# Kernel optimization log

Hardware: AMD Instinct MI355X
Metric: run time of the kernel (lower is better)

Reference implementation:

```python
import jax, jax.numpy as jnp
import numpy as np

B, N, F, H, D = 2, 2048, 1024, 16, 64


def setup_inputs() -> dict:
    key = jax.random.key(0)
    ks = jax.random.split(key, 5)
    s = 0.02
    return {
        "x": jax.random.normal(ks[0], (B, N, F), jnp.float32),
        "w_qkv": (jax.random.normal(ks[1], (3 * H * D, F), jnp.float32) * s),
        "w_out": (jax.random.normal(ks[2], (F, H * D), jnp.float32) * s),
        "w_hp_pre": (jax.random.normal(ks[3], (H, H), jnp.float32) * (1.0 / H)),
        "b_hp_pre": jnp.zeros((H,), jnp.float32),
        "w_hp_post": (jax.random.normal(ks[4], (H, H), jnp.float32) * (1.0 / H)),
        "b_hp_post": jnp.zeros((H,), jnp.float32),
    }


def reference(x, w_qkv, w_out, w_hp_pre, b_hp_pre, w_hp_post, b_hp_post):
    b, n, f = x.shape
    # qkv projection; rearrange 'b n (h d qkv) -> qkv b h n d' (qkv innermost)
    proj = (x @ w_qkv.T).reshape(b, n, H, D, 3)
    q = jnp.transpose(proj[..., 0], (0, 2, 1, 3))  # b h n d
    k = jnp.transpose(proj[..., 1], (0, 2, 1, 3))
    v = jnp.transpose(proj[..., 2], (0, 2, 1, 3))
    kv = jnp.stack([k, v], axis=0)  # (2, b, h, n, d) -- returned cache

    scale = D ** -0.5
    dots = jnp.einsum('bhid,bhjd->bhij', q, k) * scale
    # pre talking-heads: 1x1 conv over head channel
    dots = jnp.einsum('gh,bhij->bgij', w_hp_pre, dots) + b_hp_pre[None, :, None, None]
    attn = jax.nn.softmax(dots, axis=-1)
    # post talking-heads
    attn = jnp.einsum('gh,bhij->bgij', w_hp_post, attn) + b_hp_post[None, :, None, None]
    out = jnp.einsum('bhij,bhjd->bhid', attn, v)
    out = jnp.transpose(out, (0, 2, 1, 3)).reshape(b, n, H * D)
    out = out @ w_out.T
    return out, kv
```

## Files before the change

### kernel.cpp

```cpp
#include <hip/hip_runtime.h>
#include <hip/hip_bf16.h>
#include <cstdint>
#include <cstddef>

#define B_ 2
#define N_ 2048
#define F_ 1024
#define H_ 16
#define D_ 64

typedef float f32x4 __attribute__((ext_vector_type(4)));
typedef short s16x8 __attribute__((ext_vector_type(8)));
typedef short s16x4 __attribute__((ext_vector_type(4)));

__device__ __forceinline__ unsigned short f2bf(float f) {
  union { __hip_bfloat16 h; unsigned short u; } c;
  c.h = __float2bfloat16(f);
  return c.u;
}
__device__ __forceinline__ float bf2f(unsigned short u) {
  union { __hip_bfloat16 h; unsigned short u; } c;
  c.u = u;
  return __bfloat162float(c.h);
}

__global__ __launch_bounds__(256) void cvt_bf16(const float* __restrict__ in,
                                                unsigned short* __restrict__ out,
                                                int n8) {
  const int t = blockIdx.x * 256 + threadIdx.x;
  if (t >= n8) return;
  const float4* p = (const float4*)in + (size_t)t * 2;
  float4 a = p[0], b = p[1];
  s16x8 o;
  o[0] = f2bf(a.x); o[1] = f2bf(a.y); o[2] = f2bf(a.z); o[3] = f2bf(a.w);
  o[4] = f2bf(b.x); o[5] = f2bf(b.y); o[6] = f2bf(b.z); o[7] = f2bf(b.w);
  *((s16x8*)out + t) = o;
}

__global__ __launch_bounds__(256) void cvt_wqkv_perm(const float* __restrict__ in,
                                                     unsigned short* __restrict__ out) {
  const int t = blockIdx.x * 256 + threadIdx.x;
  const int rowp = t >> 7;
  const int kk = (t & 127) * 8;
  const int c = rowp >> 10, rem = rowp & 1023;
  const int h = rem >> 6, d = rem & 63;
  const float* p = in + (size_t)(h * 192 + d * 3 + c) * 1024 + kk;
  float4 a = *(const float4*)p, b = *(const float4*)(p + 4);
  s16x8 o;
  o[0] = f2bf(a.x); o[1] = f2bf(a.y); o[2] = f2bf(a.z); o[3] = f2bf(a.w);
  o[4] = f2bf(b.x); o[5] = f2bf(b.y); o[6] = f2bf(b.z); o[7] = f2bf(b.w);
  *((s16x8*)&out[(size_t)rowp * 1024 + kk]) = o;
}

__global__ __launch_bounds__(256) void cvt_sum4(const float* __restrict__ a,
                                                unsigned short* __restrict__ out) {
  const int t = blockIdx.x * 256 + threadIdx.x;
  const size_t stride = (size_t)B_ * N_ * 1024 / 4;
  float4 x0 = *((const float4*)a + t);
  float4 x1 = *((const float4*)a + stride + t);
  float4 x2 = *((const float4*)a + 2 * stride + t);
  float4 x3 = *((const float4*)a + 3 * stride + t);
  s16x4 o;
  o[0] = f2bf((x0.x + x1.x) + (x2.x + x3.x));
  o[1] = f2bf((x0.y + x1.y) + (x2.y + x3.y));
  o[2] = f2bf((x0.z + x1.z) + (x2.z + x3.z));
  o[3] = f2bf((x0.w + x1.w) + (x2.w + x3.w));
  *((s16x4*)out + t) = o;
}

template <int MODE>
__global__ __launch_bounds__(256) void gemm_bf16(const unsigned short* __restrict__ A,
                                                 const unsigned short* __restrict__ W,
                                                 float* __restrict__ o0,
                                                 unsigned short* __restrict__ oQ,
                                                 unsigned short* __restrict__ oK,
                                                 unsigned short* __restrict__ oVt) {
  __shared__ unsigned short As[128 * 72];
  __shared__ unsigned short Bs[128 * 72];
  const int m0 = blockIdx.y * 128, c0 = blockIdx.x * 128;
  const int tid = threadIdx.x;
  const int wave = tid >> 6, lane = tid & 63;
  const int wm = (wave & 1) * 64, wn = (wave >> 1) * 64;
  const int lm = lane & 15, lq = lane >> 4;
  f32x4 acc[4][4] = {};
  for (int k0 = 0; k0 < 1024; k0 += 64) {
#pragma unroll
    for (int it = 0; it < 4; ++it) {
      const int chunk = it * 256 + tid;
      const int row = chunk >> 3, kq = (chunk & 7) * 8;
      *(float4*)&As[row * 72 + kq] = *(const float4*)&A[(size_t)(m0 + row) * 1024 + k0 + kq];
      *(float4*)&Bs[row * 72 + kq] = *(const float4*)&W[(size_t)(c0 + row) * 1024 + k0 + kq];
    }
    __syncthreads();
#pragma unroll
    for (int ks = 0; ks < 2; ++ks) {
      s16x8 af[4], bfr[4];
#pragma unroll
      for (int i = 0; i < 4; ++i) {
        af[i] = *(const s16x8*)&As[(wm + i * 16 + lm) * 72 + ks * 32 + lq * 8];
        bfr[i] = *(const s16x8*)&Bs[(wn + i * 16 + lm) * 72 + ks * 32 + lq * 8];
      }
#pragma unroll
      for (int i = 0; i < 4; ++i)
#pragma unroll
        for (int j = 0; j < 4; ++j)
          acc[i][j] = __builtin_amdgcn_mfma_f32_16x16x32_bf16(af[i], bfr[j], acc[i][j], 0, 0, 0);
    }
    __syncthreads();
  }
  if (MODE == 1) {
#pragma unroll
    for (int i = 0; i < 4; ++i)
#pragma unroll
      for (int j = 0; j < 4; ++j)
#pragma unroll
        for (int r = 0; r < 4; ++r) {
          const int m = m0 + wm + i * 16 + lq * 4 + r;
          const int col = c0 + wn + j * 16 + lm;
          o0[(size_t)m * 1024 + col] = acc[i][j][r];
        }
  } else {
    const int cls = blockIdx.x >> 3;
    const int colbase = (blockIdx.x & 7) * 128;
    if (cls == 0) {
#pragma unroll
      for (int i = 0; i < 4; ++i)
#pragma unroll
        for (int j = 0; j < 4; ++j) {
          const int cl = colbase + wn + j * 16 + lm;
          const int h = cl >> 6, d = cl & 63;
#pragma unroll
          for (int r = 0; r < 4; ++r) {
            const int m = m0 + wm + i * 16 + lq * 4 + r;
            const int bb = m >> 11, n = m & 2047;
            oQ[(((size_t)bb * H_ + h) * N_ + n) * D_ + d] = f2bf(acc[i][j][r]);
          }
        }
    } else if (cls == 1) {
#pragma unroll
      for (int i = 0; i < 4; ++i)
#pragma unroll
        for (int j = 0; j < 4; ++j) {
          const int cl = colbase + wn + j * 16 + lm;
          const int h = cl >> 6, d = cl & 63;
#pragma unroll
          for (int r = 0; r < 4; ++r) {
            const int m = m0 + wm + i * 16 + lq * 4 + r;
            const int bb = m >> 11, n = m & 2047;
            const size_t idx = (((size_t)bb * H_ + h) * N_ + n) * D_ + d;
            o0[idx] = acc[i][j][r];
            oK[idx] = f2bf(acc[i][j][r]);
          }
        }
    } else {
#pragma unroll
      for (int i = 0; i < 4; ++i) {
        const int n0 = m0 + wm + i * 16 + lq * 4;
        const int bb = n0 >> 11, nl = n0 & 2047;
#pragma unroll
        for (int j = 0; j < 4; ++j) {
          const int cl = colbase + wn + j * 16 + lm;
          const int h = cl >> 6, d = cl & 63;
          s16x4 vp;
#pragma unroll
          for (int r = 0; r < 4; ++r) {
            const size_t idx = (((size_t)bb * H_ + h) * N_ + nl + r) * D_ + d;
            o0[(size_t)B_ * H_ * N_ * D_ + idx] = acc[i][j][r];
            vp[r] = (short)f2bf(acc[i][j][r]);
          }
          *(s16x4*)&oVt[(((size_t)bb * H_ + h) * D_ + d) * N_ + nl] = vp;
        }
      }
    }
  }
}

#define SS_J 20
#define SLOT 320
#define SS_I 644
#define PS_J 36
#define PS_G 1156

__global__ __launch_bounds__(512) void attn_l(const unsigned short* __restrict__ Qb,
                                              const unsigned short* __restrict__ Kb,
                                              const float* __restrict__ wpre,
                                              const float* __restrict__ bpre,
                                              float* __restrict__ l_glob) {
  __shared__ unsigned short Ssh[32 * SS_I];
  const int tid = threadIdx.x;
  const int wave = tid >> 6, lane = tid & 63;
  const int lm = lane & 15, lq = lane >> 4;
  const int b = blockIdx.z, jh = blockIdx.y;
  const int i0 = blockIdx.x * 32;
  const int j00 = jh * 512;
  const int h0 = wave * 2;

  s16x8 aq[2][2][2];
#pragma unroll
  for (int hh = 0; hh < 2; ++hh)
#pragma unroll
    for (int mi = 0; mi < 2; ++mi)
#pragma unroll
      for (int ks = 0; ks < 2; ++ks)
        aq[hh][mi][ks] = *(const s16x8*)&Qb[(((size_t)(b * H_ + h0 + hh) * N_) + i0 + mi * 16 + lm) * D_ + ks * 32 + lq * 8];

  s16x8 apre;
#pragma unroll
  for (int t = 0; t < 8; ++t) apre[t] = 0;
  if (lq < 2)
#pragma unroll
    for (int t = 0; t < 8; ++t) apre[t] = (short)f2bf(wpre[lm * 16 + lq * 8 + t] * 0.125f);
  float bpre_r[4];
#pragma unroll
  for (int r = 0; r < 4; ++r) bpre_r[r] = bpre[lq * 4 + r];

  float lacc[4][4] = {};

  for (int js = 0; js < 512; js += 32) {
    const int j0 = j00 + js;
    __syncthreads();
#pragma unroll
    for (int jt = 0; jt < 2; ++jt) {
      f32x4 c[2][2];
#pragma unroll
      for (int hh = 0; hh < 2; ++hh) {
        const unsigned short* kp = &Kb[(((size_t)(b * H_ + h0 + hh) * N_) + j0 + jt * 16 + lm) * D_ + lq * 8];
        s16x8 b0 = *(const s16x8*)kp;
        s16x8 b1 = *(const s16x8*)(kp + 32);
#pragma unroll
        for (int mi = 0; mi < 2; ++mi) {
          f32x4 cc = {};
          cc = __builtin_amdgcn_mfma_f32_16x16x32_bf16(aq[hh][mi][0], b0, cc, 0, 0, 0);
          cc = __builtin_amdgcn_mfma_f32_16x16x32_bf16(aq[hh][mi][1], b1, cc, 0, 0, 0);
          c[hh][mi] = cc;
        }
      }
#pragma unroll
      for (int mi = 0; mi < 2; ++mi)
#pragma unroll
        for (int r = 0; r < 4; ++r) {
          unsigned int pk = (unsigned int)f2bf(c[0][mi][r]) | ((unsigned int)f2bf(c[1][mi][r]) << 16);
          *(unsigned int*)&Ssh[(mi * 16 + lq * 4 + r) * SS_I + jt * SLOT + lm * SS_J + h0] = pk;
        }
    }
    __syncthreads();
#pragma unroll
    for (int ii = 0; ii < 8; ++ii) {
      const int i_loc = wave * 4 + (ii & 3), jt = ii >> 2;
      const unsigned short* srow = &Ssh[i_loc * SS_I + jt * SLOT];
      s16x8 bs;
#pragma unroll
      for (int t = 0; t < 8; ++t) bs[t] = 0;
      if (lq < 2) {
        s16x4 p0 = *(const s16x4*)(srow + lm * SS_J + lq * 8);
        s16x4 p1 = *(const s16x4*)(srow + lm * SS_J + lq * 8 + 4);
        bs[0] = p0[0]; bs[1] = p0[1]; bs[2] = p0[2]; bs[3] = p0[3];
        bs[4] = p1[0]; bs[5] = p1[1]; bs[6] = p1[2]; bs[7] = p1[3];
      }
      f32x4 c = {};
      c = __builtin_amdgcn_mfma_f32_16x16x32_bf16(apre, bs, c, 0, 0, 0);
#pragma unroll
      for (int r = 0; r < 4; ++r) lacc[ii & 3][r] += __expf(c[r] + bpre_r[r]);
    }
  }
#pragma unroll
  for (int ig = 0; ig < 4; ++ig)
#pragma unroll
    for (int r = 0; r < 4; ++r) {
      float v = lacc[ig][r];
      v += __shfl_xor(v, 1); v += __shfl_xor(v, 2);
      v += __shfl_xor(v, 4); v += __shfl_xor(v, 8);
      if (lm == 0)
        atomicAdd(&l_glob[((size_t)b * N_ + i0 + wave * 4 + ig) * H_ + lq * 4 + r], v);
    }
}

__global__ __launch_bounds__(512) void attn_av(const unsigned short* __restrict__ Qb,
                                               const unsigned short* __restrict__ Kb,
                                               const unsigned short* __restrict__ Vt,
                                               const float* __restrict__ wpre,
                                               const float* __restrict__ bpre,
                                               const float* __restrict__ wpost,
                                               const float* __restrict__ bpost,
                                               const float* __restrict__ l_glob,
                                               float* __restrict__ Opart) {
  __shared__ unsigned short Ssh[32 * SS_I];
  __shared__ unsigned short Psh[16 * PS_G];
  __shared__ float linv[512];
  const int tid = threadIdx.x;
  const int wave = tid >> 6, lane = tid & 63;
  const int lm = lane & 15, lq = lane >> 4;
  const int b = blockIdx.z, jh = blockIdx.y;
  const int i0 = blockIdx.x * 32;
  const int j00 = jh * 512;
  const int h0 = wave * 2;
  float* Oout = Opart + (size_t)jh * ((size_t)B_ * N_ * 1024);

  linv[tid] = 1.0f / l_glob[((size_t)b * N_ + i0 + (tid >> 4)) * H_ + (tid & 15)];

  s16x8 aq[2][2][2];
#pragma unroll
  for (int hh = 0; hh < 2; ++hh)
#pragma unroll
    for (int mi = 0; mi < 2; ++mi)
#pragma unroll
      for (int ks = 0; ks < 2; ++ks)
        aq[hh][mi][ks] = *(const s16x8*)&Qb[(((size_t)(b * H_ + h0 + hh) * N_) + i0 + mi * 16 + lm) * D_ + ks * 32 + lq * 8];

  s16x8 apre, apost;
#pragma unroll
  for (int t = 0; t < 8; ++t) { apre[t] = 0; apost[t] = 0; }
  if (lq < 2)
#pragma unroll
    for (int t = 0; t < 8; ++t) {
      apre[t] = (short)f2bf(wpre[lm * 16 + lq * 8 + t] * 0.125f);
      apost[t] = (short)f2bf(wpost[lm * 16 + lq * 8 + t]);
    }
  float bpre_r[4];
#pragma unroll
  for (int r = 0; r < 4; ++r) bpre_r[r] = bpre[lq * 4 + r];
  const float bpost_lm = bpost[lm];

  f32x4 acc[2][2][4] = {};

  for (int js = 0; js < 512; js += 32) {
    const int j0 = j00 + js;
#pragma unroll
    for (int jt = 0; jt < 2; ++jt) {
      f32x4 c[2][2];
#pragma unroll
      for (int hh = 0; hh < 2; ++hh) {
        const unsigned short* kp = &Kb[(((size_t)(b * H_ + h0 + hh) * N_) + j0 + jt * 16 + lm) * D_ + lq * 8];
        s16x8 b0 = *(const s16x8*)kp;
        s16x8 b1 = *(const s16x8*)(kp + 32);
#pragma unroll
        for (int mi = 0; mi < 2; ++mi) {
          f32x4 cc = {};
          cc = __builtin_amdgcn_mfma_f32_16x16x32_bf16(aq[hh][mi][0], b0, cc, 0, 0, 0);
          cc = __builtin_amdgcn_mfma_f32_16x16x32_bf16(aq[hh][mi][1], b1, cc, 0, 0, 0);
          c[hh][mi] = cc;
        }
      }
#pragma unroll
      for (int mi = 0; mi < 2; ++mi)
#pragma unroll
        for (int r = 0; r < 4; ++r) {
          unsigned int pk = (unsigned int)f2bf(c[0][mi][r]) | ((unsigned int)f2bf(c[1][mi][r]) << 16);
          *(unsigned int*)&Ssh[(mi * 16 + lq * 4 + r) * SS_I + jt * SLOT + lm * SS_J + h0] = pk;
        }
    }
    __syncthreads();
#pragma unroll
    for (int ii = 0; ii < 8; ++ii) {
      const int i_loc = wave * 4 + (ii & 3), jt = ii >> 2;
      unsigned short* srow = &Ssh[i_loc * SS_I + jt * SLOT];
      s16x8 bs;
#pragma unroll
      for (int t = 0; t < 8; ++t) bs[t] = 0;
      if (lq < 2) {
        s16x4 p0 = *(const s16x4*)(srow + lm * SS_J + lq * 8);
        s16x4 p1 = *(const s16x4*)(srow + lm * SS_J + lq * 8 + 4);
        bs[0] = p0[0]; bs[1] = p0[1]; bs[2] = p0[2]; bs[3] = p0[3];
        bs[4] = p1[0]; bs[5] = p1[1]; bs[6] = p1[2]; bs[7] = p1[3];
      }
      f32x4 c = {};
      c = __builtin_amdgcn_mfma_f32_16x16x32_bf16(apre, bs, c, 0, 0, 0);
      const float4 li = *(const float4*)&linv[i_loc * 16 + lq * 4];
      const float lif[4] = {li.x, li.y, li.z, li.w};
      s16x4 ep;
#pragma unroll
      for (int r = 0; r < 4; ++r)
        ep[r] = (short)f2bf(__expf(c[r] + bpre_r[r]) * lif[r]);
      *(s16x4*)(srow + lm * SS_J + lq * 4) = ep;
      s16x8 be;
#pragma unroll
      for (int t = 0; t < 8; ++t) be[t] = 0;
      if (lq < 2) {
        s16x4 q0 = *(const s16x4*)(srow + lm * SS_J + lq * 8);
        s16x4 q1 = *(const s16x4*)(srow + lm * SS_J + lq * 8 + 4);
        be[0] = q0[0]; be[1] = q0[1]; be[2] = q0[2]; be[3] = q0[3];
        be[4] = q1[0]; be[5] = q1[1]; be[6] = q1[2]; be[7] = q1[3];
      }
      f32x4 c2 = {};
      c2 = __builtin_amdgcn_mfma_f32_16x16x32_bf16(be, apost, c2, 0, 0, 0);
      s16x4 pv;
#pragma unroll
      for (int r = 0; r < 4; ++r) pv[r] = (short)f2bf(c2[r] + bpost_lm);
      *(s16x4*)&Psh[lm * PS_G + i_loc * PS_J + jt * 16 + lq * 4] = pv;
    }
    __syncthreads();
#pragma unroll
    for (int g = 0; g < 2; ++g) {
      const int gg = h0 + g;
      s16x8 bv[4];
#pragma unroll
      for (int nd = 0; nd < 4; ++nd)
        bv[nd] = *(const s16x8*)&Vt[(((size_t)(b * H_ + gg) * D_) + nd * 16 + lm) * N_ + j0 + lq * 8];
#pragma unroll
      for (int mi = 0; mi < 2; ++mi) {
        const unsigned short* pb = &Psh[gg * PS_G + (mi * 16 + lm) * PS_J + lq * 8];
        s16x4 a0 = *(const s16x4*)pb;
        s16x4 a1 = *(const s16x4*)(pb + 4);
        s16x8 ap;
        ap[0] = a0[0]; ap[1] = a0[1]; ap[2] = a0[2]; ap[3] = a0[3];
        ap[4] = a1[0]; ap[5] = a1[1]; ap[6] = a1[2]; ap[7] = a1[3];
#pragma unroll
        for (int nd = 0; nd < 4; ++nd)
          acc[g][mi][nd] = __builtin_amdgcn_mfma_f32_16x16x32_bf16(ap, bv[nd], acc[g][mi][nd], 0, 0, 0);
      }
    }
  }
#pragma unroll
  for (int g = 0; g < 2; ++g)
#pragma unroll
    for (int mi = 0; mi < 2; ++mi)
#pragma unroll
      for (int nd = 0; nd < 4; ++nd)
#pragma unroll
        for (int r = 0; r < 4; ++r)
          Oout[((size_t)b * N_ + i0 + mi * 16 + lq * 4 + r) * 1024 + (h0 + g) * 64 + nd * 16 + lm] = acc[g][mi][nd][r];
}

extern "C" void kernel_launch(void* const* d_in, const int* in_sizes, int n_in,
                              void* d_out, int out_size, void* d_ws,
                              size_t ws_size, hipStream_t stream) {
  (void)in_sizes; (void)n_in; (void)out_size; (void)ws_size;
  const float* x      = (const float*)d_in[0];
  const float* w_qkv  = (const float*)d_in[1];
  const float* w_out  = (const float*)d_in[2];
  const float* w_pre  = (const float*)d_in[3];
  const float* b_pre  = (const float*)d_in[4];
  const float* w_post = (const float*)d_in[5];
  const float* b_post = (const float*)d_in[6];

  float* out = (float*)d_out;
  float* kv  = out + (size_t)B_ * N_ * F_;

  unsigned short* xb  = (unsigned short*)d_ws;
  unsigned short* wqb = xb + (size_t)4096 * 1024;
  unsigned short* wob = wqb + (size_t)3072 * 1024;
  unsigned short* Qb  = wob + (size_t)1024 * 1024;
  unsigned short* Kb  = Qb + (size_t)B_ * H_ * N_ * D_;
  unsigned short* Vt  = Kb + (size_t)B_ * H_ * N_ * D_;
  unsigned short* O1  = Vt + (size_t)B_ * H_ * N_ * D_;
  float* l_glob = (float*)(O1 + (size_t)B_ * N_ * F_);
  float* Oh = l_glob + (size_t)B_ * N_ * H_;

  cvt_bf16<<<dim3(4096 * 1024 / 8 / 256), 256, 0, stream>>>(x, xb, 4096 * 1024 / 8);
  cvt_wqkv_perm<<<dim3(3072 * 128 / 256), 256, 0, stream>>>(w_qkv, wqb);
  cvt_bf16<<<dim3(1024 * 1024 / 8 / 256), 256, 0, stream>>>(w_out, wob, 1024 * 1024 / 8);
  hipMemsetAsync(l_glob, 0, (size_t)B_ * N_ * H_ * 4, stream);

  gemm_bf16<0><<<dim3(3072 / 128, 4096 / 128), 256, 0, stream>>>(xb, wqb, kv, Qb, Kb, Vt);

  attn_l<<<dim3(N_ / 32, 4, B_), 512, 0, stream>>>(Qb, Kb, w_pre, b_pre, l_glob);
  attn_av<<<dim3(N_ / 32, 4, B_), 512, 0, stream>>>(Qb, Kb, Vt, w_pre, b_pre, w_post, b_post,
                                                    l_glob, Oh);

  cvt_sum4<<<dim3(B_ * N_ * F_ / 4 / 256), 256, 0, stream>>>(Oh, O1);

  gemm_bf16<1><<<dim3(1024 / 128, 4096 / 128), 256, 0, stream>>>(O1, wob, out, nullptr, nullptr, nullptr);
}
```

Before: 440.0 us.

## Halve attention query tile to 16 rows and raise occupancy with zero-padded LDS

Both attention kernels now process 16 query rows per block instead of 32, doubling the grid, shrinking LDS and register footprint, and requesting four blocks per CU via launch bounds. The talking-heads MFMA operands are no longer zeroed conditionally per lane: the LDS score buffer is zero-initialized once, so all lanes load unconditionally. LDS reads, MFMAs and exps are batched into separate phases. The aim is better latency hiding through occupancy, at the cost of reloading K and V tiles twice as often per query row.

```diff
diff --git a/kernel.cpp b/kernel.cpp
--- a/kernel.cpp
+++ b/kernel.cpp
@@ -178,31 +178,32 @@
 #define SS_J 20
 #define SLOT 320
 #define SS_I 644
+#define SS_TOT (16 * SS_I + 16)
 #define PS_J 36
-#define PS_G 1156
-
-__global__ __launch_bounds__(512) void attn_l(const unsigned short* __restrict__ Qb,
-                                              const unsigned short* __restrict__ Kb,
-                                              const float* __restrict__ wpre,
-                                              const float* __restrict__ bpre,
-                                              float* __restrict__ l_glob) {
-  __shared__ unsigned short Ssh[32 * SS_I];
+#define PS_G 580
+
+__global__ __launch_bounds__(512, 4) void attn_l(const unsigned short* __restrict__ Qb,
+                                                 const unsigned short* __restrict__ Kb,
+                                                 const float* __restrict__ wpre,
+                                                 const float* __restrict__ bpre,
+                                                 float* __restrict__ l_glob) {
+  __shared__ unsigned short Ssh[SS_TOT];
   const int tid = threadIdx.x;
   const int wave = tid >> 6, lane = tid & 63;
   const int lm = lane & 15, lq = lane >> 4;
   const int b = blockIdx.z, jh = blockIdx.y;
-  const int i0 = blockIdx.x * 32;
+  const int i0 = blockIdx.x * 16;
   const int j00 = jh * 512;
   const int h0 = wave * 2;
 
-  s16x8 aq[2][2][2];
+  for (int t = tid; t < SS_TOT; t += 512) Ssh[t] = 0;
+
+  s16x8 aq[2][2];
 #pragma unroll
   for (int hh = 0; hh < 2; ++hh)
 #pragma unroll
-    for (int mi = 0; mi < 2; ++mi)
-#pragma unroll
-      for (int ks = 0; ks < 2; ++ks)
-        aq[hh][mi][ks] = *(const s16x8*)&Qb[(((size_t)(b * H_ + h0 + hh) * N_) + i0 + mi * 16 + lm) * D_ + ks * 32 + lq * 8];
+    for (int ks = 0; ks < 2; ++ks)
+      aq[hh][ks] = *(const s16x8*)&Qb[(((size_t)(b * H_ + h0 + hh) * N_) + i0 + lm) * D_ + ks * 32 + lq * 8];
 
   s16x8 apre;
 #pragma unroll
@@ -214,98 +215,92 @@
 #pragma unroll
   for (int r = 0; r < 4; ++r) bpre_r[r] = bpre[lq * 4 + r];
 
-  float lacc[4][4] = {};
+  float lacc[2][4] = {};
 
   for (int js = 0; js < 512; js += 32) {
     const int j0 = j00 + js;
     __syncthreads();
 #pragma unroll
     for (int jt = 0; jt < 2; ++jt) {
-      f32x4 c[2][2];
+      f32x4 c[2];
 #pragma unroll
       for (int hh = 0; hh < 2; ++hh) {
         const unsigned short* kp = &Kb[(((size_t)(b * H_ + h0 + hh) * N_) + j0 + jt * 16 + lm) * D_ + lq * 8];
         s16x8 b0 = *(const s16x8*)kp;
         s16x8 b1 = *(const s16x8*)(kp + 32);
-#pragma unroll
-        for (int mi = 0; mi < 2; ++mi) {
-          f32x4 cc = {};
-          cc = __builtin_amdgcn_mfma_f32_16x16x32_bf16(aq[hh][mi][0], b0, cc, 0, 0, 0);
-          cc = __builtin_amdgcn_mfma_f32_16x16x32_bf16(aq[hh][mi][1], b1, cc, 0, 0, 0);
-          c[hh][mi] = cc;
-        }
-      }
-#pragma unroll
-      for (int mi = 0; mi < 2; ++mi)
-#pragma unroll
-        for (int r = 0; r < 4; ++r) {
-          unsigned int pk = (unsigned int)f2bf(c[0][mi][r]) | ((unsigned int)f2bf(c[1][mi][r]) << 16);
-          *(unsigned int*)&Ssh[(mi * 16 + lq * 4 + r) * SS_I + jt * SLOT + lm * SS_J + h0] = pk;
-        }
-    }
-    __syncthreads();
-#pragma unroll
-    for (int ii = 0; ii < 8; ++ii) {
-      const int i_loc = wave * 4 + (ii & 3), jt = ii >> 2;
-      const unsigned short* srow = &Ssh[i_loc * SS_I + jt * SLOT];
+        f32x4 cc = {};
+        cc = __builtin_amdgcn_mfma_f32_16x16x32_bf16(aq[hh][0], b0, cc, 0, 0, 0);
+        cc = __builtin_amdgcn_mfma_f32_16x16x32_bf16(aq[hh][1], b1, cc, 0, 0, 0);
+        c[hh] = cc;
+      }
+#pragma unroll
+      for (int r = 0; r < 4; ++r) {
+        unsigned int pk = (unsigned int)f2bf(c[0][r]) | ((unsigned int)f2bf(c[1][r]) << 16);
+        *(unsigned int*)&Ssh[(lq * 4 + r) * SS_I + jt * SLOT + lm * SS_J + h0] = pk;
+      }
+    }
+    __syncthreads();
+    s16x4 p0[4], p1[4];
+#pragma unroll
+    for (int ii = 0; ii < 4; ++ii) {
+      const unsigned short* srow = &Ssh[(wave * 2 + (ii & 1)) * SS_I + (ii >> 1) * SLOT + lm * SS_J + lq * 8];
+      p0[ii] = *(const s16x4*)srow;
+      p1[ii] = *(const s16x4*)(srow + 4);
+    }
+#pragma unroll
+    for (int ii = 0; ii < 4; ++ii) {
       s16x8 bs;
-#pragma unroll
-      for (int t = 0; t < 8; ++t) bs[t] = 0;
-      if (lq < 2) {
-        s16x4 p0 = *(const s16x4*)(srow + lm * SS_J + lq * 8);
-        s16x4 p1 = *(const s16x4*)(srow + lm * SS_J + lq * 8 + 4);
-        bs[0] = p0[0]; bs[1] = p0[1]; bs[2] = p0[2]; bs[3] = p0[3];
-        bs[4] = p1[0]; bs[5] = p1[1]; bs[6] = p1[2]; bs[7] = p1[3];
-      }
+      bs[0] = p0[ii][0]; bs[1] = p0[ii][1]; bs[2] = p0[ii][2]; bs[3] = p0[ii][3];
+      bs[4] = p1[ii][0]; bs[5] = p1[ii][1]; bs[6] = p1[ii][2]; bs[7] = p1[ii][3];
       f32x4 c = {};
       c = __builtin_amdgcn_mfma_f32_16x16x32_bf16(apre, bs, c, 0, 0, 0);
 #pragma unroll
-      for (int r = 0; r < 4; ++r) lacc[ii & 3][r] += __expf(c[r] + bpre_r[r]);
+      for (int r = 0; r < 4; ++r) lacc[ii & 1][r] += __expf(c[r] + bpre_r[r]);
     }
   }
 #pragma unroll
-  for (int ig = 0; ig < 4; ++ig)
+  for (int ig = 0; ig < 2; ++ig)
 #pragma unroll
     for (int r = 0; r < 4; ++r) {
       float v = lacc[ig][r];
       v += __shfl_xor(v, 1); v += __shfl_xor(v, 2);
       v += __shfl_xor(v, 4); v += __shfl_xor(v, 8);
       if (lm == 0)
-        atomicAdd(&l_glob[((size_t)b * N_ + i0 + wave * 4 + ig) * H_ + lq * 4 + r], v);
-    }
-}
-
-__global__ __launch_bounds__(512) void attn_av(const unsigned short* __restrict__ Qb,
-                                               const unsigned short* __restrict__ Kb,
-                                               const unsigned short* __restrict__ Vt,
-                                               const float* __restrict__ wpre,
-                                               const float* __restrict__ bpre,
-                                               const float* __restrict__ wpost,
-                                               const float* __restrict__ bpost,
-                                               const float* __restrict__ l_glob,
-                                               float* __restrict__ Opart) {
-  __shared__ unsigned short Ssh[32 * SS_I];
+        atomicAdd(&l_glob[((size_t)b * N_ + i0 + wave * 2 + ig) * H_ + lq * 4 + r], v);
+    }
+}
+
+__global__ __launch_bounds__(512, 4) void attn_av(const unsigned short* __restrict__ Qb,
+                                                  const unsigned short* __restrict__ Kb,
+                                                  const unsigned short* __restrict__ Vt,
+                                                  const float* __restrict__ wpre,
+                                                  const float* __restrict__ bpre,
+                                                  const float* __restrict__ wpost,
+                                                  const float* __restrict__ bpost,
+                                                  const float* __restrict__ l_glob,
+                                                  float* __restrict__ Opart) {
+  __shared__ unsigned short Ssh[SS_TOT];
   __shared__ unsigned short Psh[16 * PS_G];
-  __shared__ float linv[512];
+  __shared__ float linv[256];
   const int tid = threadIdx.x;
   const int wave = tid >> 6, lane = tid & 63;
   const int lm = lane & 15, lq = lane >> 4;
   const int b = blockIdx.z, jh = blockIdx.y;
-  const int i0 = blockIdx.x * 32;
+  const int i0 = blockIdx.x * 16;
   const int j00 = jh * 512;
   const int h0 = wave * 2;
   float* Oout = Opart + (size_t)jh * ((size_t)B_ * N_ * 1024);
 
-  linv[tid] = 1.0f / l_glob[((size_t)b * N_ + i0 + (tid >> 4)) * H_ + (tid & 15)];
-
-  s16x8 aq[2][2][2];
+  for (int t = tid; t < SS_TOT; t += 512) Ssh[t] = 0;
+  if (tid < 256)
+    linv[tid] = 1.0f / l_glob[((size_t)b * N_ + i0 + (tid >> 4)) * H_ + (tid & 15)];
+
+  s16x8 aq[2][2];
 #pragma unroll
   for (int hh = 0; hh < 2; ++hh)
 #pragma unroll
-    for (int mi = 0; mi < 2; ++mi)
-#pragma unroll
-      for (int ks = 0; ks < 2; ++ks)
-        aq[hh][mi][ks] = *(const s16x8*)&Qb[(((size_t)(b * H_ + h0 + hh) * N_) + i0 + mi * 16 + lm) * D_ + ks * 32 + lq * 8];
+    for (int ks = 0; ks < 2; ++ks)
+      aq[hh][ks] = *(const s16x8*)&Qb[(((size_t)(b * H_ + h0 + hh) * N_) + i0 + lm) * D_ + ks * 32 + lq * 8];
 
   s16x8 apre, apost;
 #pragma unroll
@@ -321,72 +316,82 @@
   for (int r = 0; r < 4; ++r) bpre_r[r] = bpre[lq * 4 + r];
   const float bpost_lm = bpost[lm];
 
-  f32x4 acc[2][2][4] = {};
+  __syncthreads();
+
+  float lifs[2][4];
+#pragma unroll
+  for (int u = 0; u < 2; ++u)
+#pragma unroll
+    for (int r = 0; r < 4; ++r)
+      lifs[u][r] = linv[(wave * 2 + u) * 16 + lq * 4 + r];
+
+  f32x4 acc[2][4] = {};
 
   for (int js = 0; js < 512; js += 32) {
     const int j0 = j00 + js;
 #pragma unroll
     for (int jt = 0; jt < 2; ++jt) {
-      f32x4 c[2][2];
+      f32x4 c[2];
 #pragma unroll
       for (int hh = 0; hh < 2; ++hh) {
         const unsigned short* kp = &Kb[(((size_t)(b * H_ + h0 + hh) * N_) + j0 + jt * 16 + lm) * D_ + lq * 8];
         s16x8 b0 = *(const s16x8*)kp;
         s16x8 b1 = *(const s16x8*)(kp + 32);
-#pragma unroll
-        for (int mi = 0; mi < 2; ++mi) {
-          f32x4 cc = {};
-          cc = __builtin_amdgcn_mfma_f32_16x16x32_bf16(aq[hh][mi][0], b0, cc, 0, 0, 0);
-          cc = __builtin_amdgcn_mfma_f32_16x16x32_bf16(aq[hh][mi][1], b1, cc, 0, 0, 0);
-          c[hh][mi] = cc;
-        }
-      }
-#pragma unroll
-      for (int mi = 0; mi < 2; ++mi)
-#pragma unroll
-        for (int r = 0; r < 4; ++r) {
-          unsigned int pk = (unsigned int)f2bf(c[0][mi][r]) | ((unsigned int)f2bf(c[1][mi][r]) << 16);
-          *(unsigned int*)&Ssh[(mi * 16 + lq * 4 + r) * SS_I + jt * SLOT + lm * SS_J + h0] = pk;
-        }
-    }
-    __syncthreads();
-#pragma unroll
-    for (int ii = 0; ii < 8; ++ii) {
-      const int i_loc = wave * 4 + (ii & 3), jt = ii >> 2;
-      unsigned short* srow = &Ssh[i_loc * SS_I + jt * SLOT];
+        f32x4 cc = {};
+        cc = __builtin_amdgcn_mfma_f32_16x16x32_bf16(aq[hh][0], b0, cc, 0, 0, 0);
+        cc = __builtin_amdgcn_mfma_f32_16x16x32_bf16(aq[hh][1], b1, cc, 0, 0, 0);
+        c[hh] = cc;
+      }
+#pragma unroll
+      for (int r = 0; r < 4; ++r) {
+        unsigned int pk = (unsigned int)f2bf(c[0][r]) | ((unsigned int)f2bf(c[1][r]) << 16);
+        *(unsigned int*)&Ssh[(lq * 4 + r) * SS_I + jt * SLOT + lm * SS_J + h0] = pk;
+      }
+    }
+    __syncthreads();
+    s16x4 p0[4], p1[4];
+#pragma unroll
+    for (int ii = 0; ii < 4; ++ii) {
+      const unsigned short* srow = &Ssh[(wave * 2 + (ii & 1)) * SS_I + (ii >> 1) * SLOT + lm * SS_J + lq * 8];
+      p0[ii] = *(const s16x4*)srow;
+      p1[ii] = *(const s16x4*)(srow + 4);
+    }
+    f32x4 cpre[4];
+#pragma unroll
+    for (int ii = 0; ii < 4; ++ii) {
       s16x8 bs;
-#pragma unroll
-      for (int t = 0; t < 8; ++t) bs[t] = 0;
-      if (lq < 2) {
-        s16x4 p0 = *(const s16x4*)(srow + lm * SS_J + lq * 8);
-        s16x4 p1 = *(const s16x4*)(srow + lm * SS_J + lq * 8 + 4);
-        bs[0] = p0[0]; bs[1] = p0[1]; bs[2] = p0[2]; bs[3] = p0[3];
-        bs[4] = p1[0]; bs[5] = p1[1]; bs[6] = p1[2]; bs[7] = p1[3];
-      }
+      bs[0] = p0[ii][0]; bs[1] = p0[ii][1]; bs[2] = p0[ii][2]; bs[3] = p0[ii][3];
+      bs[4] = p1[ii][0]; bs[5] = p1[ii][1]; bs[6] = p1[ii][2]; bs[7] = p1[ii][3];
       f32x4 c = {};
-      c = __builtin_amdgcn_mfma_f32_16x16x32_bf16(apre, bs, c, 0, 0, 0);
-      const float4 li = *(const float4*)&linv[i_loc * 16 + lq * 4];
-      const float lif[4] = {li.x, li.y, li.z, li.w};
+      cpre[ii] = __builtin_amdgcn_mfma_f32_16x16x32_bf16(apre, bs, c, 0, 0, 0);
+    }
+#pragma unroll
+    for (int ii = 0; ii < 4; ++ii) {
+      unsigned short* srow = &Ssh[(wave * 2 + (ii & 1)) * SS_I + (ii >> 1) * SLOT];
       s16x4 ep;
 #pragma unroll
       for (int r = 0; r < 4; ++r)
-        ep[r] = (short)f2bf(__expf(c[r] + bpre_r[r]) * lif[r]);
+        ep[r] = (short)f2bf(__expf(cpre[ii][r] + bpre_r[r]) * lifs[ii & 1][r]);
       *(s16x4*)(srow + lm * SS_J + lq * 4) = ep;
+    }
+    s16x4 q0[4], q1[4];
+#pragma unroll
+    for (int ii = 0; ii < 4; ++ii) {
+      const unsigned short* srow = &Ssh[(wave * 2 + (ii & 1)) * SS_I + (ii >> 1) * SLOT + lm * SS_J + lq * 8];
+      q0[ii] = *(const s16x4*)srow;
+      q1[ii] = *(const s16x4*)(srow + 4);
+    }
+#pragma unroll
+    for (int ii = 0; ii < 4; ++ii) {
       s16x8 be;
-#pragma unroll
-      for (int t = 0; t < 8; ++t) be[t] = 0;
-      if (lq < 2) {
-        s16x4 q0 = *(const s16x4*)(srow + lm * SS_J + lq * 8);
-        s16x4 q1 = *(const s16x4*)(srow + lm * SS_J + lq * 8 + 4);
-        be[0] = q0[0]; be[1] = q0[1]; be[2] = q0[2]; be[3] = q0[3];
-        be[4] = q1[0]; be[5] = q1[1]; be[6] = q1[2]; be[7] = q1[3];
-      }
+      be[0] = q0[ii][0]; be[1] = q0[ii][1]; be[2] = q0[ii][2]; be[3] = q0[ii][3];
+      be[4] = q1[ii][0]; be[5] = q1[ii][1]; be[6] = q1[ii][2]; be[7] = q1[ii][3];
       f32x4 c2 = {};
       c2 = __builtin_amdgcn_mfma_f32_16x16x32_bf16(be, apost, c2, 0, 0, 0);
       s16x4 pv;
 #pragma unroll
       for (int r = 0; r < 4; ++r) pv[r] = (short)f2bf(c2[r] + bpost_lm);
-      *(s16x4*)&Psh[lm * PS_G + i_loc * PS_J + jt * 16 + lq * 4] = pv;
+      *(s16x4*)&Psh[lm * PS_G + (wave * 2 + (ii & 1)) * PS_J + (ii >> 1) * 16 + lq * 4] = pv;
     }
     __syncthreads();
 #pragma unroll
@@ -396,29 +401,24 @@
 #pragma unroll
       for (int nd = 0; nd < 4; ++nd)
         bv[nd] = *(const s16x8*)&Vt[(((size_t)(b * H_ + gg) * D_) + nd * 16 + lm) * N_ + j0 + lq * 8];
-#pragma unroll
-      for (int mi = 0; mi < 2; ++mi) {
-        const unsigned short* pb = &Psh[gg * PS_G + (mi * 16 + lm) * PS_J + lq * 8];
-        s16x4 a0 = *(const s16x4*)pb;
-        s16x4 a1 = *(const s16x4*)(pb + 4);
-        s16x8 ap;
-        ap[0] = a0[0]; ap[1] = a0[1]; ap[2] = a0[2]; ap[3] = a0[3];
-        ap[4] = a1[0]; ap[5] = a1[1]; ap[6] = a1[2]; ap[7] = a1[3];
-#pragma unroll
-        for (int nd = 0; nd < 4; ++nd)
-          acc[g][mi][nd] = __builtin_amdgcn_mfma_f32_16x16x32_bf16(ap, bv[nd], acc[g][mi][nd], 0, 0, 0);
-      }
+      const unsigned short* pb = &Psh[gg * PS_G + lm * PS_J + lq * 8];
+      s16x4 a0 = *(const s16x4*)pb;
+      s16x4 a1 = *(const s16x4*)(pb + 4);
+      s16x8 ap;
+      ap[0] = a0[0]; ap[1] = a0[1]; ap[2] = a0[2]; ap[3] = a0[3];
+      ap[4] = a1[0]; ap[5] = a1[1]; ap[6] = a1[2]; ap[7] = a1[3];
+#pragma unroll
+      for (int nd = 0; nd < 4; ++nd)
+        acc[g][nd] = __builtin_amdgcn_mfma_f32_16x16x32_bf16(ap, bv[nd], acc[g][nd], 0, 0, 0);
     }
   }
 #pragma unroll
   for (int g = 0; g < 2; ++g)
 #pragma unroll
-    for (int mi = 0; mi < 2; ++mi)
-#pragma unroll
-      for (int nd = 0; nd < 4; ++nd)
-#pragma unroll
-        for (int r = 0; r < 4; ++r)
-          Oout[((size_t)b * N_ + i0 + mi * 16 + lq * 4 + r) * 1024 + (h0 + g) * 64 + nd * 16 + lm] = acc[g][mi][nd][r];
+    for (int nd = 0; nd < 4; ++nd)
+#pragma unroll
+      for (int r = 0; r < 4; ++r)
+        Oout[((size_t)b * N_ + i0 + lq * 4 + r) * 1024 + (h0 + g) * 64 + nd * 16 + lm] = acc[g][nd][r];
 }
 
 extern "C" void kernel_launch(void* const* d_in, const int* in_sizes, int n_in,
@@ -453,8 +453,8 @@
 
   gemm_bf16<0><<<dim3(3072 / 128, 4096 / 128), 256, 0, stream>>>(xb, wqb, kv, Qb, Kb, Vt);
 
-  attn_l<<<dim3(N_ / 32, 4, B_), 512, 0, stream>>>(Qb, Kb, w_pre, b_pre, l_glob);
-  attn_av<<<dim3(N_ / 32, 4, B_), 512, 0, stream>>>(Qb, Kb, Vt, w_pre, b_pre, w_post, b_post,
+  attn_l<<<dim3(N_ / 16, 4, B_), 512, 0, stream>>>(Qb, Kb, w_pre, b_pre, l_glob);
+  attn_av<<<dim3(N_ / 16, 4, B_), 512, 0, stream>>>(Qb, Kb, Vt, w_pre, b_pre, w_post, b_post,
                                                     l_glob, Oh);
 
   cvt_sum4<<<dim3(B_ * N_ * F_ / 4 / 256), 256, 0, stream>>>(Oh, O1);
```

After: 549.6 us. 1.25x slower.

## Raise occupancy in attention kernels by reloading Q and batching LDS reads

Applied to the files above, without the earlier changes.

Drops the register-resident Q fragments and reloads them from global memory inside the inner loop, and adds launch_bounds min-block hints (6 and 4) to cut register use and raise occupancy. The shared S buffer is padded and zero-filled up front so the lq>=2 lanes can read it unconditionally, removing the branchy zeroing. The pre/post talking-head loops are restructured to batch four LDS reads before the MFMAs, exposing more instruction-level parallelism. The cost is extra global/L2 traffic for Q on every tile and possible register spills under the tighter bounds.

```diff
diff --git a/kernel.cpp b/kernel.cpp
--- a/kernel.cpp
+++ b/kernel.cpp
@@ -178,15 +178,16 @@
 #define SS_J 20
 #define SLOT 320
 #define SS_I 644
+#define SS_TOT (32 * SS_I + 16)
 #define PS_J 36
 #define PS_G 1156
 
-__global__ __launch_bounds__(512) void attn_l(const unsigned short* __restrict__ Qb,
-                                              const unsigned short* __restrict__ Kb,
-                                              const float* __restrict__ wpre,
-                                              const float* __restrict__ bpre,
-                                              float* __restrict__ l_glob) {
-  __shared__ unsigned short Ssh[32 * SS_I];
+__global__ __launch_bounds__(512, 6) void attn_l(const unsigned short* __restrict__ Qb,
+                                                 const unsigned short* __restrict__ Kb,
+                                                 const float* __restrict__ wpre,
+                                                 const float* __restrict__ bpre,
+                                                 float* __restrict__ l_glob) {
+  __shared__ unsigned short Ssh[SS_TOT];
   const int tid = threadIdx.x;
   const int wave = tid >> 6, lane = tid & 63;
   const int lm = lane & 15, lq = lane >> 4;
@@ -195,14 +196,7 @@
   const int j00 = jh * 512;
   const int h0 = wave * 2;
 
-  s16x8 aq[2][2][2];
-#pragma unroll
-  for (int hh = 0; hh < 2; ++hh)
-#pragma unroll
-    for (int mi = 0; mi < 2; ++mi)
-#pragma unroll
-      for (int ks = 0; ks < 2; ++ks)
-        aq[hh][mi][ks] = *(const s16x8*)&Qb[(((size_t)(b * H_ + h0 + hh) * N_) + i0 + mi * 16 + lm) * D_ + ks * 32 + lq * 8];
+  for (int t = tid; t < SS_TOT; t += 512) Ssh[t] = 0;
 
   s16x8 apre;
 #pragma unroll
@@ -229,9 +223,12 @@
         s16x8 b1 = *(const s16x8*)(kp + 32);
 #pragma unroll
         for (int mi = 0; mi < 2; ++mi) {
+          const unsigned short* qp = &Qb[(((size_t)(b * H_ + h0 + hh) * N_) + i0 + mi * 16 + lm) * D_ + lq * 8];
+          s16x8 a0 = *(const s16x8*)qp;
+          s16x8 a1 = *(const s16x8*)(qp + 32);
           f32x4 cc = {};
-          cc = __builtin_amdgcn_mfma_f32_16x16x32_bf16(aq[hh][mi][0], b0, cc, 0, 0, 0);
-          cc = __builtin_amdgcn_mfma_f32_16x16x32_bf16(aq[hh][mi][1], b1, cc, 0, 0, 0);
+          cc = __builtin_amdgcn_mfma_f32_16x16x32_bf16(a0, b0, cc, 0, 0, 0);
+          cc = __builtin_amdgcn_mfma_f32_16x16x32_bf16(a1, b1, cc, 0, 0, 0);
           c[hh][mi] = cc;
         }
       }
@@ -245,22 +242,24 @@
     }
     __syncthreads();
 #pragma unroll
-    for (int ii = 0; ii < 8; ++ii) {
-      const int i_loc = wave * 4 + (ii & 3), jt = ii >> 2;
-      const unsigned short* srow = &Ssh[i_loc * SS_I + jt * SLOT];
-      s16x8 bs;
-#pragma unroll
-      for (int t = 0; t < 8; ++t) bs[t] = 0;
-      if (lq < 2) {
-        s16x4 p0 = *(const s16x4*)(srow + lm * SS_J + lq * 8);
-        s16x4 p1 = *(const s16x4*)(srow + lm * SS_J + lq * 8 + 4);
-        bs[0] = p0[0]; bs[1] = p0[1]; bs[2] = p0[2]; bs[3] = p0[3];
-        bs[4] = p1[0]; bs[5] = p1[1]; bs[6] = p1[2]; bs[7] = p1[3];
-      }
-      f32x4 c = {};
-      c = __builtin_amdgcn_mfma_f32_16x16x32_bf16(apre, bs, c, 0, 0, 0);
-#pragma unroll
-      for (int r = 0; r < 4; ++r) lacc[ii & 3][r] += __expf(c[r] + bpre_r[r]);
+    for (int jt = 0; jt < 2; ++jt) {
+      s16x4 p0[4], p1[4];
+#pragma unroll
+      for (int u = 0; u < 4; ++u) {
+        const unsigned short* srow = &Ssh[(wave * 4 + u) * SS_I + jt * SLOT + lm * SS_J + lq * 8];
+        p0[u] = *(const s16x4*)srow;
+        p1[u] = *(const s16x4*)(srow + 4);
+      }
+#pragma unroll
+      for (int u = 0; u < 4; ++u) {
+        s16x8 bs;
+        bs[0] = p0[u][0]; bs[1] = p0[u][1]; bs[2] = p0[u][2]; bs[3] = p0[u][3];
+        bs[4] = p1[u][0]; bs[5] = p1[u][1]; bs[6] = p1[u][2]; bs[7] = p1[u][3];
+        f32x4 c = {};
+        c = __builtin_amdgcn_mfma_f32_16x16x32_bf16(apre, bs, c, 0, 0, 0);
+#pragma unroll
+        for (int r = 0; r < 4; ++r) lacc[u][r] += __expf(c[r] + bpre_r[r]);
+      }
     }
   }
 #pragma unroll
@@ -275,16 +274,16 @@
     }
 }
 
-__global__ __launch_bounds__(512) void attn_av(const unsigned short* __restrict__ Qb,
-                                               const unsigned short* __restrict__ Kb,
-                                               const unsigned short* __restrict__ Vt,
-                                               const float* __restrict__ wpre,
-                                               const float* __restrict__ bpre,
-                                               const float* __restrict__ wpost,
-                                               const float* __restrict__ bpost,
-                                               const float* __restrict__ l_glob,
-                                               float* __restrict__ Opart) {
-  __shared__ unsigned short Ssh[32 * SS_I];
+__global__ __launch_bounds__(512, 4) void attn_av(const unsigned short* __restrict__ Qb,
+                                                  const unsigned short* __restrict__ Kb,
+                                                  const unsigned short* __restrict__ Vt,
+                                                  const float* __restrict__ wpre,
+                                                  const float* __restrict__ bpre,
+                                                  const float* __restrict__ wpost,
+                                                  const float* __restrict__ bpost,
+                                                  const float* __restrict__ l_glob,
+                                                  float* __restrict__ Opart) {
+  __shared__ unsigned short Ssh[SS_TOT];
   __shared__ unsigned short Psh[16 * PS_G];
   __shared__ float linv[512];
   const int tid = threadIdx.x;
@@ -296,16 +295,8 @@
   const int h0 = wave * 2;
   float* Oout = Opart + (size_t)jh * ((size_t)B_ * N_ * 1024);
 
+  for (int t = tid; t < SS_TOT; t += 512) Ssh[t] = 0;
   linv[tid] = 1.0f / l_glob[((size_t)b * N_ + i0 + (tid >> 4)) * H_ + (tid & 15)];
-
-  s16x8 aq[2][2][2];
-#pragma unroll
-  for (int hh = 0; hh < 2; ++hh)
-#pragma unroll
-    for (int mi = 0; mi < 2; ++mi)
-#pragma unroll
-      for (int ks = 0; ks < 2; ++ks)
-        aq[hh][mi][ks] = *(const s16x8*)&Qb[(((size_t)(b * H_ + h0 + hh) * N_) + i0 + mi * 16 + lm) * D_ + ks * 32 + lq * 8];
 
   s16x8 apre, apost;
 #pragma unroll
@@ -320,6 +311,8 @@
 #pragma unroll
   for (int r = 0; r < 4; ++r) bpre_r[r] = bpre[lq * 4 + r];
   const float bpost_lm = bpost[lm];
+
+  __syncthreads();
 
   f32x4 acc[2][2][4] = {};
 
@@ -335,9 +328,12 @@
         s16x8 b1 = *(const s16x8*)(kp + 32);
 #pragma unroll
         for (int mi = 0; mi < 2; ++mi) {
+          const unsigned short* qp = &Qb[(((size_t)(b * H_ + h0 + hh) * N_) + i0 + mi * 16 + lm) * D_ + lq * 8];
+          s16x8 a0 = *(const s16x8*)qp;
+          s16x8 a1 = *(const s16x8*)(qp + 32);
           f32x4 cc = {};
-          cc = __builtin_amdgcn_mfma_f32_16x16x32_bf16(aq[hh][mi][0], b0, cc, 0, 0, 0);
-          cc = __builtin_amdgcn_mfma_f32_16x16x32_bf16(aq[hh][mi][1], b1, cc, 0, 0, 0);
+          cc = __builtin_amdgcn_mfma_f32_16x16x32_bf16(a0, b0, cc, 0, 0, 0);
+          cc = __builtin_amdgcn_mfma_f32_16x16x32_bf16(a1, b1, cc, 0, 0, 0);
           c[hh][mi] = cc;
         }
       }
@@ -351,42 +347,54 @@
     }
     __syncthreads();
 #pragma unroll
-    for (int ii = 0; ii < 8; ++ii) {
-      const int i_loc = wave * 4 + (ii & 3), jt = ii >> 2;
-      unsigned short* srow = &Ssh[i_loc * SS_I + jt * SLOT];
-      s16x8 bs;
-#pragma unroll
-      for (int t = 0; t < 8; ++t) bs[t] = 0;
-      if (lq < 2) {
-        s16x4 p0 = *(const s16x4*)(srow + lm * SS_J + lq * 8);
-        s16x4 p1 = *(const s16x4*)(srow + lm * SS_J + lq * 8 + 4);
-        bs[0] = p0[0]; bs[1] = p0[1]; bs[2] = p0[2]; bs[3] = p0[3];
-        bs[4] = p1[0]; bs[5] = p1[1]; bs[6] = p1[2]; bs[7] = p1[3];
-      }
-      f32x4 c = {};
-      c = __builtin_amdgcn_mfma_f32_16x16x32_bf16(apre, bs, c, 0, 0, 0);
-      const float4 li = *(const float4*)&linv[i_loc * 16 + lq * 4];
-      const float lif[4] = {li.x, li.y, li.z, li.w};
-      s16x4 ep;
-#pragma unroll
-      for (int r = 0; r < 4; ++r)
-        ep[r] = (short)f2bf(__expf(c[r] + bpre_r[r]) * lif[r]);
-      *(s16x4*)(srow + lm * SS_J + lq * 4) = ep;
-      s16x8 be;
-#pragma unroll
-      for (int t = 0; t < 8; ++t) be[t] = 0;
-      if (lq < 2) {
-        s16x4 q0 = *(const s16x4*)(srow + lm * SS_J + lq * 8);
-        s16x4 q1 = *(const s16x4*)(srow + lm * SS_J + lq * 8 + 4);
-        be[0] = q0[0]; be[1] = q0[1]; be[2] = q0[2]; be[3] = q0[3];
-        be[4] = q1[0]; be[5] = q1[1]; be[6] = q1[2]; be[7] = q1[3];
-      }
-      f32x4 c2 = {};
-      c2 = __builtin_amdgcn_mfma_f32_16x16x32_bf16(be, apost, c2, 0, 0, 0);
-      s16x4 pv;
-#pragma unroll
-      for (int r = 0; r < 4; ++r) pv[r] = (short)f2bf(c2[r] + bpost_lm);
-      *(s16x4*)&Psh[lm * PS_G + i_loc * PS_J + jt * 16 + lq * 4] = pv;
+    for (int jt = 0; jt < 2; ++jt) {
+      s16x4 p0[4], p1[4];
+#pragma unroll
+      for (int u = 0; u < 4; ++u) {
+        const unsigned short* srow = &Ssh[(wave * 4 + u) * SS_I + jt * SLOT + lm * SS_J + lq * 8];
+        p0[u] = *(const s16x4*)srow;
+        p1[u] = *(const s16x4*)(srow + 4);
+      }
+      f32x4 cpre[4];
+#pragma unroll
+      for (int u = 0; u < 4; ++u) {
+        s16x8 bs;
+        bs[0] = p0[u][0]; bs[1] = p0[u][1]; bs[2] = p0[u][2]; bs[3] = p0[u][3];
+        bs[4] = p1[u][0]; bs[5] = p1[u][1]; bs[6] = p1[u][2]; bs[7] = p1[u][3];
+        f32x4 c = {};
+        cpre[u] = __builtin_amdgcn_mfma_f32_16x16x32_bf16(apre, bs, c, 0, 0, 0);
+      }
+#pragma unroll
+      for (int u = 0; u < 4; ++u) {
+        const int i_loc = wave * 4 + u;
+        unsigned short* srow = &Ssh[i_loc * SS_I + jt * SLOT];
+        const float4 li = *(const float4*)&linv[i_loc * 16 + lq * 4];
+        const float lif[4] = {li.x, li.y, li.z, li.w};
+        s16x4 ep;
+#pragma unroll
+        for (int r = 0; r < 4; ++r)
+          ep[r] = (short)f2bf(__expf(cpre[u][r] + bpre_r[r]) * lif[r]);
+        *(s16x4*)(srow + lm * SS_J + lq * 4) = ep;
+      }
+      s16x4 q0[4], q1[4];
+#pragma unroll
+      for (int u = 0; u < 4; ++u) {
+        const unsigned short* srow = &Ssh[(wave * 4 + u) * SS_I + jt * SLOT + lm * SS_J + lq * 8];
+        q0[u] = *(const s16x4*)srow;
+        q1[u] = *(const s16x4*)(srow + 4);
+      }
+#pragma unroll
+      for (int u = 0; u < 4; ++u) {
+        s16x8 be;
+        be[0] = q0[u][0]; be[1] = q0[u][1]; be[2] = q0[u][2]; be[3] = q0[u][3];
+        be[4] = q1[u][0]; be[5] = q1[u][1]; be[6] = q1[u][2]; be[7] = q1[u][3];
+        f32x4 c2 = {};
+        c2 = __builtin_amdgcn_mfma_f32_16x16x32_bf16(be, apost, c2, 0, 0, 0);
+        s16x4 pv;
+#pragma unroll
+        for (int r = 0; r < 4; ++r) pv[r] = (short)f2bf(c2[r] + bpost_lm);
+        *(s16x4*)&Psh[lm * PS_G + (wave * 4 + u) * PS_J + jt * 16 + lq * 4] = pv;
+      }
     }
     __syncthreads();
 #pragma unroll
```

After: 628.8 us. 1.43x slower.
